# Optimization experiments

Measured on AMD Instinct MI355X. Metric: run time of the kernel, lower is better.

The kernel has to match this reference:

```python
import jax, jax.numpy as jnp
import numpy as np

N_NODES = 10000
N_EDGES = 640000
D = 128
N_GRAPHS = 16
N_CLASSES = 10


def setup_inputs() -> dict:
    key = jax.random.key(0)
    ks = jax.random.split(key, 12)
    x = jax.random.normal(ks[0], (N_NODES, D), dtype=jnp.float32)
    edge_index = jax.random.randint(ks[1], (2, N_EDGES), 0, N_NODES, dtype=jnp.int64)
    batch_ids = jnp.sort(jax.random.randint(ks[2], (N_NODES,), 0, N_GRAPHS, dtype=jnp.int64))
    s = 1.0 / np.sqrt(D)
    W_in = jax.random.normal(ks[3], (D, D), dtype=jnp.float32) * s
    W_self = jax.random.normal(ks[4], (D, D), dtype=jnp.float32) * s
    b = jnp.zeros((D,), dtype=jnp.float32)
    W_e1 = jax.random.normal(ks[5], (2 * D, D), dtype=jnp.float32) * (1.0 / np.sqrt(2 * D))
    b_e1 = jnp.zeros((D,), dtype=jnp.float32)
    W_e2 = jax.random.normal(ks[6], (D, 1), dtype=jnp.float32) * s
    b_e2 = jnp.zeros((1,), dtype=jnp.float32)
    W_cls = jax.random.normal(ks[7], (D, N_CLASSES), dtype=jnp.float32) * s
    b_cls = jnp.zeros((N_CLASSES,), dtype=jnp.float32)
    return {"x": x, "edge_index": edge_index, "batch_ids": batch_ids,
            "W_in": W_in, "W_self": W_self, "b": b,
            "W_e1": W_e1, "b_e1": b_e1, "W_e2": W_e2, "b_e2": b_e2,
            "W_cls": W_cls, "b_cls": b_cls}


def reference(x, edge_index, batch_ids, W_in, W_self, b, W_e1, b_e1, W_e2, b_e2, W_cls, b_cls):
    src, dst = edge_index[0], edge_index[1]
    # --- gnn(data) -> (z_node, z_graph) : GCN-style message passing ---
    h = x @ W_in                                  # [N, D]
    agg = jax.ops.segment_sum(h[src], dst, num_segments=N_NODES)  # [N, D]
    z_node = jax.nn.relu(agg + x @ W_self + b)    # [N, D]
    # mean pool per graph -> z_graph [B, D]
    sums = jax.ops.segment_sum(z_node, batch_ids, num_segments=N_GRAPHS)
    counts = jax.ops.segment_sum(jnp.ones((N_NODES,), dtype=z_node.dtype), batch_ids, num_segments=N_GRAPHS)
    z_graph = sums / jnp.maximum(counts, 1.0)[:, None]
    # --- edge predictor: gather, concat, MLP ---
    edge_features = jnp.concatenate([z_node[src], z_node[dst]], axis=1)  # [E, 2D]
    pred_edge = jax.nn.relu(edge_features @ W_e1 + b_e1) @ W_e2 + b_e2   # [E, 1]
    # --- classifier ---
    pred_class = z_graph @ W_cls + b_cls          # [B, n_classes]
    return (pred_edge, pred_class)
```

## Files before the change

### kernel.cpp

```cpp
#include <hip/hip_runtime.h>

#define N_NODES   10000
#define N_EDGES   640000
#define DIM       128
#define N_GRAPHS  16
#define N_CLASSES 10

typedef unsigned int uint;
typedef unsigned short ushort;

__device__ __forceinline__ float bf2f(uint lo16) {
    return __uint_as_float(lo16 << 16);
}
__device__ __forceinline__ ushort f2bf(float f) {
    uint u = __float_as_uint(f);
    u += 0x7fffu + ((u >> 16) & 1u);
    return (ushort)(u >> 16);
}

__global__ __launch_bounds__(256) void conv_bf16(
    const float* __restrict__ x, uint* __restrict__ xb)
{
    const int idx = blockIdx.x * 256 + threadIdx.x;
    const float4 v = ((const float4*)x)[idx];
    uint lo = (uint)f2bf(v.x) | ((uint)f2bf(v.y) << 16);
    uint hi = (uint)f2bf(v.z) | ((uint)f2bf(v.w) << 16);
    ((uint2*)xb)[idx] = make_uint2(lo, hi);
}

__global__ __launch_bounds__(256) void hist_dst(
    const int* __restrict__ dst, int* __restrict__ cnt)
{
    const int base = (blockIdx.x * 256 + threadIdx.x) * 4;
    const int d0 = dst[base + 0];
    const int d1 = dst[base + 1];
    const int d2 = dst[base + 2];
    const int d3 = dst[base + 3];
    atomicAdd(&cnt[d0], 1);
    atomicAdd(&cnt[d1], 1);
    atomicAdd(&cnt[d2], 1);
    atomicAdd(&cnt[d3], 1);
}

__global__ __launch_bounds__(256) void count_nodes(
    const int* __restrict__ bid, float* __restrict__ gcnt)
{
    __shared__ int h[N_GRAPHS];
    const int t = threadIdx.x;
    if (t < N_GRAPHS) h[t] = 0;
    __syncthreads();
    for (int n = t; n < N_NODES; n += 256) atomicAdd(&h[bid[n]], 1);
    __syncthreads();
    if (t < N_GRAPHS) gcnt[t] = (float)h[t];
}

__global__ __launch_bounds__(1024) void scan_k(
    const int* __restrict__ cnt, int* __restrict__ cursor)
{
    __shared__ int s[1024];
    const int t = threadIdx.x;
    int local[10];
    int sum = 0;
    if (t < 1000) {
        for (int j = 0; j < 10; ++j) { local[j] = sum; sum += cnt[t * 10 + j]; }
    }
    s[t] = (t < 1000) ? sum : 0;
    __syncthreads();
    for (int st = 1; st < 1024; st <<= 1) {
        int v = (t >= st) ? s[t - st] : 0;
        __syncthreads();
        s[t] += v;
        __syncthreads();
    }
    if (t < 1000) {
        const int off = (t == 0) ? 0 : s[t - 1];
        for (int j = 0; j < 10; ++j) cursor[t * 10 + j] = off + local[j];
    }
}

__global__ __launch_bounds__(256) void fill_csr(
    const int* __restrict__ src, const int* __restrict__ dst,
    int* __restrict__ cursor, uint* __restrict__ srcs)
{
    const int base = (blockIdx.x * 256 + threadIdx.x) * 4;
    const int d0 = dst[base + 0];
    const int d1 = dst[base + 1];
    const int d2 = dst[base + 2];
    const int d3 = dst[base + 3];
    const int s0 = src[base + 0];
    const int s1 = src[base + 1];
    const int s2 = src[base + 2];
    const int s3 = src[base + 3];
    const int p0 = atomicAdd(&cursor[d0], 1);
    const int p1 = atomicAdd(&cursor[d1], 1);
    const int p2 = atomicAdd(&cursor[d2], 1);
    const int p3 = atomicAdd(&cursor[d3], 1);
    srcs[p0] = (uint)s0;
    srcs[p1] = (uint)s1;
    srcs[p2] = (uint)s2;
    srcs[p3] = (uint)s3;
}

__global__ __launch_bounds__(256) void gather_xb(
    const uint* __restrict__ xb,
    const int* __restrict__ cnt, const int* __restrict__ cursor,
    const uint* __restrict__ srcs,
    float* __restrict__ XAGG)
{
    const int n    = blockIdx.x * 4 + (threadIdx.x >> 6);
    const int lane = threadIdx.x & 63;
    const int end  = cursor[n];
    int i = end - cnt[n];

    float a0 = 0.f, b0 = 0.f, a1 = 0.f, b1 = 0.f;
    float a2 = 0.f, b2 = 0.f, a3 = 0.f, b3 = 0.f;

    for (; i + 4 <= end; i += 4) {
        const uint s0 = srcs[i], s1 = srcs[i + 1], s2 = srcs[i + 2], s3 = srcs[i + 3];
        const uint v0 = xb[s0 * 64 + lane];
        const uint v1 = xb[s1 * 64 + lane];
        const uint v2 = xb[s2 * 64 + lane];
        const uint v3 = xb[s3 * 64 + lane];
        a0 += bf2f(v0 & 0xffffu); b0 += bf2f(v0 >> 16);
        a1 += bf2f(v1 & 0xffffu); b1 += bf2f(v1 >> 16);
        a2 += bf2f(v2 & 0xffffu); b2 += bf2f(v2 >> 16);
        a3 += bf2f(v3 & 0xffffu); b3 += bf2f(v3 >> 16);
    }
    for (; i < end; ++i) {
        const uint v = xb[srcs[i] * 64 + lane];
        a0 += bf2f(v & 0xffffu); b0 += bf2f(v >> 16);
    }
    float2 s;
    s.x = (a0 + a1) + (a2 + a3);
    s.y = (b0 + b1) + (b2 + b3);
    *(float2*)&XAGG[n * DIM + lane * 2] = s;
}

__global__ __launch_bounds__(256) void gemm_zu(
    const float* __restrict__ XAGG_in, const float* __restrict__ x,
    const float* __restrict__ W_in, const float* __restrict__ W_self,
    const float* __restrict__ b, const int* __restrict__ bid,
    const float* __restrict__ W_e1, const float* __restrict__ b_e1,
    float* __restrict__ gsum, ushort* __restrict__ U12)
{
    __shared__ float sa[16 * DIM];
    __shared__ float sb[16 * DIM];
    __shared__ int sbid[16];
    const int base = blockIdx.x * 16;
    const int t = threadIdx.x;
    {
        const float4* ga = (const float4*)(XAGG_in + base * DIM);
        const float4* gb = (const float4*)(x + base * DIM);
        float4* la = (float4*)sa;
        float4* lb = (float4*)sb;
        for (int i = t; i < 16 * DIM / 4; i += 256) { la[i] = ga[i]; lb[i] = gb[i]; }
        if (t < 16) sbid[t] = bid[base + t];
    }
    __syncthreads();

    const int half = t >> 7, c = t & 127;

    {
        const float* __restrict__ W = half ? W_self : W_in;
        const float4* A4 = (const float4*)(half ? sb : sa);
        float acc[16];
#pragma unroll
        for (int r = 0; r < 16; ++r) acc[r] = 0.f;
        for (int k4 = 0; k4 < DIM / 4; ++k4) {
            const float w0 = W[(k4 * 4 + 0) * DIM + c];
            const float w1 = W[(k4 * 4 + 1) * DIM + c];
            const float w2 = W[(k4 * 4 + 2) * DIM + c];
            const float w3 = W[(k4 * 4 + 3) * DIM + c];
#pragma unroll
            for (int r = 0; r < 16; ++r) {
                const float4 xv = A4[r * (DIM / 4) + k4];
                acc[r] = fmaf(xv.x, w0, acc[r]);
                acc[r] = fmaf(xv.y, w1, acc[r]);
                acc[r] = fmaf(xv.z, w2, acc[r]);
                acc[r] = fmaf(xv.w, w3, acc[r]);
            }
        }
        __syncthreads();
        if (half) {
#pragma unroll
            for (int r = 0; r < 16; ++r) sb[r * DIM + c] = acc[r];
        }
        __syncthreads();
        if (!half) {
            const float bv = b[c];
            float run = 0.f;
            int cur = sbid[0];
#pragma unroll
            for (int r = 0; r < 16; ++r) {
                const float z = fmaxf(acc[r] + sb[r * DIM + c] + bv, 0.f);
                sa[r * DIM + c] = z;
                const int g = sbid[r];
                if (g != cur) { unsafeAtomicAdd(&gsum[cur * DIM + c], run); run = 0.f; cur = g; }
                run += z;
            }
            unsafeAtomicAdd(&gsum[cur * DIM + c], run);
        }
        __syncthreads();
    }

    {
        const float* __restrict__ W = W_e1 + half * 128 * DIM;
        const float4* Z4 = (const float4*)sa;
        float acc[16];
#pragma unroll
        for (int r = 0; r < 16; ++r) acc[r] = 0.f;
        for (int k4 = 0; k4 < DIM / 4; ++k4) {
            const float w0 = W[(k4 * 4 + 0) * DIM + c];
            const float w1 = W[(k4 * 4 + 1) * DIM + c];
            const float w2 = W[(k4 * 4 + 2) * DIM + c];
            const float w3 = W[(k4 * 4 + 3) * DIM + c];
#pragma unroll
            for (int r = 0; r < 16; ++r) {
                const float4 xv = Z4[r * (DIM / 4) + k4];
                acc[r] = fmaf(xv.x, w0, acc[r]);
                acc[r] = fmaf(xv.y, w1, acc[r]);
                acc[r] = fmaf(xv.z, w2, acc[r]);
                acc[r] = fmaf(xv.w, w3, acc[r]);
            }
        }
        const float bv = half ? 0.f : b_e1[c];
        for (int r = 0; r < 16; ++r)
            U12[(base + r) * 256 + half * 128 + c] = f2bf(acc[r] + bv);
    }
}

__device__ __forceinline__ void ch2(uint a, uint b, float wl, float wh,
                                    float& accl, float& acch)
{
    const float fl = fmaxf(__uint_as_float(a << 16) + __uint_as_float(b << 16), 0.f);
    const float fh = fmaxf(__uint_as_float(a & 0xffff0000u) + __uint_as_float(b & 0xffff0000u), 0.f);
    accl = fmaf(fl, wl, accl);
    acch = fmaf(fh, wh, acch);
}

__global__ __launch_bounds__(256) void edge_mlp3(
    const ushort* __restrict__ U12,
    const int* __restrict__ src, const int* __restrict__ dst,
    const float* __restrict__ W_e2, const float* __restrict__ b_e2,
    float* __restrict__ out)
{
    __shared__ float ws[DIM];
    const int t = threadIdx.x;
    if (t < DIM) ws[t] = W_e2[t];
    __syncthreads();

    const int l16  = t & 15;
    const int grp  = t >> 4;
    const int e    = blockIdx.x * 16 + grp;

    const int s = src[e];
    const int d = dst[e];

    const uint4 a  = *(const uint4*)(U12 + s * 256 + l16 * 8);
    const uint4 bv = *(const uint4*)(U12 + d * 256 + 128 + l16 * 8);
    const float4 w0 = ((const float4*)ws)[l16 * 2 + 0];
    const float4 w1 = ((const float4*)ws)[l16 * 2 + 1];

    float acc0 = 0.f, acc1 = 0.f;
    ch2(a.x, bv.x, w0.x, w0.y, acc0, acc1);
    ch2(a.y, bv.y, w0.z, w0.w, acc0, acc1);
    ch2(a.z, bv.z, w1.x, w1.y, acc0, acc1);
    ch2(a.w, bv.w, w1.z, w1.w, acc0, acc1);

    float p = acc0 + acc1;
#pragma unroll
    for (int off = 8; off >= 1; off >>= 1)
        p += __shfl_xor(p, off);

    if (l16 == 0) out[e] = p + b_e2[0];
}

__global__ __launch_bounds__(256) void classify(
    const float* __restrict__ gsum, const float* __restrict__ gcnt,
    const float* __restrict__ W_cls, const float* __restrict__ b_cls,
    float* __restrict__ out)
{
    const int t = threadIdx.x;
    if (t >= N_GRAPHS * N_CLASSES) return;
    const int g = t / N_CLASSES;
    const int c = t % N_CLASSES;
    const float inv = 1.0f / fmaxf(gcnt[g], 1.0f);
    float acc = 0.f;
    for (int k = 0; k < DIM; ++k)
        acc += gsum[g * DIM + k] * W_cls[k * N_CLASSES + c];
    out[g * N_CLASSES + c] = acc * inv + b_cls[c];
}

extern "C" void kernel_launch(void* const* d_in, const int* in_sizes, int n_in,
                              void* d_out, int out_size, void* d_ws, size_t ws_size,
                              hipStream_t stream)
{
    const float* x      = (const float*)d_in[0];
    const int*   eidx   = (const int*)  d_in[1];
    const int*   bid    = (const int*)  d_in[2];
    const float* W_in   = (const float*)d_in[3];
    const float* W_self = (const float*)d_in[4];
    const float* b      = (const float*)d_in[5];
    const float* W_e1   = (const float*)d_in[6];
    const float* b_e1   = (const float*)d_in[7];
    const float* W_e2   = (const float*)d_in[8];
    const float* b_e2   = (const float*)d_in[9];
    const float* W_cls  = (const float*)d_in[10];
    const float* b_cls  = (const float*)d_in[11];
    float* out = (float*)d_out;

    char* ws = (char*)d_ws;
    int*    cnt    = (int*)   (ws);
    float*  gsum   = (float*) (ws + 40960);
    float*  gcnt   = (float*) (ws + 49152);
    int*    cursor = (int*)   (ws + 65536);
    uint*   srcs   = (uint*)  (ws + 131072);
    float*  XAGG   = (float*) (ws + 131072 + 2560000);
    ushort* U12    = (ushort*)(ws + 131072 + 7680000);
    uint*   xb     = (uint*)  (ws + 131072 + 12800000);

    const int* src = eidx;
    const int* dst = eidx + N_EDGES;

    hipMemsetAsync(d_ws, 0, 65536, stream);

    conv_bf16  <<<(N_NODES * DIM / 4) / 256, 256, 0, stream>>>(x, xb);
    hist_dst   <<<N_EDGES / 1024, 256, 0, stream>>>(dst, cnt);
    count_nodes<<<1, 256, 0, stream>>>(bid, gcnt);
    scan_k     <<<1, 1024, 0, stream>>>(cnt, cursor);
    fill_csr   <<<N_EDGES / 1024, 256, 0, stream>>>(src, dst, cursor, srcs);
    gather_xb  <<<N_NODES / 4, 256, 0, stream>>>(xb, cnt, cursor, srcs, XAGG);
    gemm_zu    <<<N_NODES / 16, 256, 0, stream>>>(XAGG, x, W_in, W_self, b, bid,
                                                  W_e1, b_e1, gsum, U12);
    edge_mlp3  <<<N_EDGES / 16, 256, 0, stream>>>(U12, src, dst, W_e2, b_e2, out);
    classify   <<<1, 256, 0, stream>>>(gsum, gcnt, W_cls, b_cls, out + N_EDGES);
}
```

Baseline: 280.9 us.

## Traverse edges in dst-sorted CSR order for edge MLP and shrink gemm tile

fill_csr now stores (src, original edge id) pairs, and the edge MLP runs per destination node. It loads the node's U2 row once and walks its incoming edges, writing each result scattered back to the original edge index. The aim is to drop the random dst-row gather and get reuse of U2. The gather loop is unrolled to 8, and gemm_zu uses 8 rows per block for more blocks. The costs are a doubled index array, scattered output writes, and per-node load imbalance with only 625 blocks in the edge kernel.

```diff
diff --git a/kernel.cpp b/kernel.cpp
--- a/kernel.cpp
+++ b/kernel.cpp
@@ -80,7 +80,7 @@
 
 __global__ __launch_bounds__(256) void fill_csr(
     const int* __restrict__ src, const int* __restrict__ dst,
-    int* __restrict__ cursor, uint* __restrict__ srcs)
+    int* __restrict__ cursor, uint2* __restrict__ pairs)
 {
     const int base = (blockIdx.x * 256 + threadIdx.x) * 4;
     const int d0 = dst[base + 0];
@@ -95,16 +95,16 @@
     const int p1 = atomicAdd(&cursor[d1], 1);
     const int p2 = atomicAdd(&cursor[d2], 1);
     const int p3 = atomicAdd(&cursor[d3], 1);
-    srcs[p0] = (uint)s0;
-    srcs[p1] = (uint)s1;
-    srcs[p2] = (uint)s2;
-    srcs[p3] = (uint)s3;
+    pairs[p0] = make_uint2((uint)s0, (uint)(base + 0));
+    pairs[p1] = make_uint2((uint)s1, (uint)(base + 1));
+    pairs[p2] = make_uint2((uint)s2, (uint)(base + 2));
+    pairs[p3] = make_uint2((uint)s3, (uint)(base + 3));
 }
 
 __global__ __launch_bounds__(256) void gather_xb(
     const uint* __restrict__ xb,
     const int* __restrict__ cnt, const int* __restrict__ cursor,
-    const uint* __restrict__ srcs,
+    const uint2* __restrict__ pairs,
     float* __restrict__ XAGG)
 {
     const int n    = blockIdx.x * 4 + (threadIdx.x >> 6);
@@ -115,19 +115,26 @@
     float a0 = 0.f, b0 = 0.f, a1 = 0.f, b1 = 0.f;
     float a2 = 0.f, b2 = 0.f, a3 = 0.f, b3 = 0.f;
 
-    for (; i + 4 <= end; i += 4) {
-        const uint s0 = srcs[i], s1 = srcs[i + 1], s2 = srcs[i + 2], s3 = srcs[i + 3];
-        const uint v0 = xb[s0 * 64 + lane];
-        const uint v1 = xb[s1 * 64 + lane];
-        const uint v2 = xb[s2 * 64 + lane];
-        const uint v3 = xb[s3 * 64 + lane];
+    for (; i + 8 <= end; i += 8) {
+        const uint v0 = xb[pairs[i + 0].x * 64 + lane];
+        const uint v1 = xb[pairs[i + 1].x * 64 + lane];
+        const uint v2 = xb[pairs[i + 2].x * 64 + lane];
+        const uint v3 = xb[pairs[i + 3].x * 64 + lane];
+        const uint v4 = xb[pairs[i + 4].x * 64 + lane];
+        const uint v5 = xb[pairs[i + 5].x * 64 + lane];
+        const uint v6 = xb[pairs[i + 6].x * 64 + lane];
+        const uint v7 = xb[pairs[i + 7].x * 64 + lane];
         a0 += bf2f(v0 & 0xffffu); b0 += bf2f(v0 >> 16);
         a1 += bf2f(v1 & 0xffffu); b1 += bf2f(v1 >> 16);
         a2 += bf2f(v2 & 0xffffu); b2 += bf2f(v2 >> 16);
         a3 += bf2f(v3 & 0xffffu); b3 += bf2f(v3 >> 16);
+        a0 += bf2f(v4 & 0xffffu); b0 += bf2f(v4 >> 16);
+        a1 += bf2f(v5 & 0xffffu); b1 += bf2f(v5 >> 16);
+        a2 += bf2f(v6 & 0xffffu); b2 += bf2f(v6 >> 16);
+        a3 += bf2f(v7 & 0xffffu); b3 += bf2f(v7 >> 16);
     }
     for (; i < end; ++i) {
-        const uint v = xb[srcs[i] * 64 + lane];
+        const uint v = xb[pairs[i].x * 64 + lane];
         a0 += bf2f(v & 0xffffu); b0 += bf2f(v >> 16);
     }
     float2 s;
@@ -136,6 +143,7 @@
     *(float2*)&XAGG[n * DIM + lane * 2] = s;
 }
 
+#define ZROWS 8
 __global__ __launch_bounds__(256) void gemm_zu(
     const float* __restrict__ XAGG_in, const float* __restrict__ x,
     const float* __restrict__ W_in, const float* __restrict__ W_self,
@@ -143,18 +151,18 @@
     const float* __restrict__ W_e1, const float* __restrict__ b_e1,
     float* __restrict__ gsum, ushort* __restrict__ U12)
 {
-    __shared__ float sa[16 * DIM];
-    __shared__ float sb[16 * DIM];
-    __shared__ int sbid[16];
-    const int base = blockIdx.x * 16;
+    __shared__ float sa[ZROWS * DIM];
+    __shared__ float sb[ZROWS * DIM];
+    __shared__ int sbid[ZROWS];
+    const int base = blockIdx.x * ZROWS;
     const int t = threadIdx.x;
     {
         const float4* ga = (const float4*)(XAGG_in + base * DIM);
         const float4* gb = (const float4*)(x + base * DIM);
         float4* la = (float4*)sa;
         float4* lb = (float4*)sb;
-        for (int i = t; i < 16 * DIM / 4; i += 256) { la[i] = ga[i]; lb[i] = gb[i]; }
-        if (t < 16) sbid[t] = bid[base + t];
+        for (int i = t; i < ZROWS * DIM / 4; i += 256) { la[i] = ga[i]; lb[i] = gb[i]; }
+        if (t < ZROWS) sbid[t] = bid[base + t];
     }
     __syncthreads();
 
@@ -163,16 +171,16 @@
     {
         const float* __restrict__ W = half ? W_self : W_in;
         const float4* A4 = (const float4*)(half ? sb : sa);
-        float acc[16];
-#pragma unroll
-        for (int r = 0; r < 16; ++r) acc[r] = 0.f;
+        float acc[ZROWS];
+#pragma unroll
+        for (int r = 0; r < ZROWS; ++r) acc[r] = 0.f;
         for (int k4 = 0; k4 < DIM / 4; ++k4) {
             const float w0 = W[(k4 * 4 + 0) * DIM + c];
             const float w1 = W[(k4 * 4 + 1) * DIM + c];
             const float w2 = W[(k4 * 4 + 2) * DIM + c];
             const float w3 = W[(k4 * 4 + 3) * DIM + c];
 #pragma unroll
-            for (int r = 0; r < 16; ++r) {
+            for (int r = 0; r < ZROWS; ++r) {
                 const float4 xv = A4[r * (DIM / 4) + k4];
                 acc[r] = fmaf(xv.x, w0, acc[r]);
                 acc[r] = fmaf(xv.y, w1, acc[r]);
@@ -183,7 +191,7 @@
         __syncthreads();
         if (half) {
 #pragma unroll
-            for (int r = 0; r < 16; ++r) sb[r * DIM + c] = acc[r];
+            for (int r = 0; r < ZROWS; ++r) sb[r * DIM + c] = acc[r];
         }
         __syncthreads();
         if (!half) {
@@ -191,7 +199,7 @@
             float run = 0.f;
             int cur = sbid[0];
 #pragma unroll
-            for (int r = 0; r < 16; ++r) {
+            for (int r = 0; r < ZROWS; ++r) {
                 const float z = fmaxf(acc[r] + sb[r * DIM + c] + bv, 0.f);
                 sa[r * DIM + c] = z;
                 const int g = sbid[r];
@@ -206,16 +214,16 @@
     {
         const float* __restrict__ W = W_e1 + half * 128 * DIM;
         const float4* Z4 = (const float4*)sa;
-        float acc[16];
-#pragma unroll
-        for (int r = 0; r < 16; ++r) acc[r] = 0.f;
+        float acc[ZROWS];
+#pragma unroll
+        for (int r = 0; r < ZROWS; ++r) acc[r] = 0.f;
         for (int k4 = 0; k4 < DIM / 4; ++k4) {
             const float w0 = W[(k4 * 4 + 0) * DIM + c];
             const float w1 = W[(k4 * 4 + 1) * DIM + c];
             const float w2 = W[(k4 * 4 + 2) * DIM + c];
             const float w3 = W[(k4 * 4 + 3) * DIM + c];
 #pragma unroll
-            for (int r = 0; r < 16; ++r) {
+            for (int r = 0; r < ZROWS; ++r) {
                 const float4 xv = Z4[r * (DIM / 4) + k4];
                 acc[r] = fmaf(xv.x, w0, acc[r]);
                 acc[r] = fmaf(xv.y, w1, acc[r]);
@@ -224,7 +232,7 @@
             }
         }
         const float bv = half ? 0.f : b_e1[c];
-        for (int r = 0; r < 16; ++r)
+        for (int r = 0; r < ZROWS; ++r)
             U12[(base + r) * 256 + half * 128 + c] = f2bf(acc[r] + bv);
     }
 }
@@ -238,9 +246,10 @@
     acch = fmaf(fh, wh, acch);
 }
 
-__global__ __launch_bounds__(256) void edge_mlp3(
+__global__ __launch_bounds__(256) void edge_mlp4(
     const ushort* __restrict__ U12,
-    const int* __restrict__ src, const int* __restrict__ dst,
+    const int* __restrict__ cnt, const int* __restrict__ cursor,
+    const uint2* __restrict__ pairs,
     const float* __restrict__ W_e2, const float* __restrict__ b_e2,
     float* __restrict__ out)
 {
@@ -249,30 +258,55 @@
     if (t < DIM) ws[t] = W_e2[t];
     __syncthreads();
 
-    const int l16  = t & 15;
-    const int grp  = t >> 4;
-    const int e    = blockIdx.x * 16 + grp;
-
-    const int s = src[e];
-    const int d = dst[e];
-
-    const uint4 a  = *(const uint4*)(U12 + s * 256 + l16 * 8);
-    const uint4 bv = *(const uint4*)(U12 + d * 256 + 128 + l16 * 8);
+    const int l16 = t & 15;
+    const int grp = t >> 4;
+    const int n   = blockIdx.x * 16 + grp;
+
+    const int end = cursor[n];
+    int i = end - cnt[n];
+
+    const uint4 u2 = *(const uint4*)(U12 + n * 256 + 128 + l16 * 8);
     const float4 w0 = ((const float4*)ws)[l16 * 2 + 0];
     const float4 w1 = ((const float4*)ws)[l16 * 2 + 1];
-
-    float acc0 = 0.f, acc1 = 0.f;
-    ch2(a.x, bv.x, w0.x, w0.y, acc0, acc1);
-    ch2(a.y, bv.y, w0.z, w0.w, acc0, acc1);
-    ch2(a.z, bv.z, w1.x, w1.y, acc0, acc1);
-    ch2(a.w, bv.w, w1.z, w1.w, acc0, acc1);
-
-    float p = acc0 + acc1;
-#pragma unroll
-    for (int off = 8; off >= 1; off >>= 1)
-        p += __shfl_xor(p, off);
-
-    if (l16 == 0) out[e] = p + b_e2[0];
+    const float be2 = b_e2[0];
+
+    for (; i + 2 <= end; i += 2) {
+        const uint2 pa = pairs[i];
+        const uint2 pb = pairs[i + 1];
+        const uint4 A = *(const uint4*)(U12 + pa.x * 256 + l16 * 8);
+        const uint4 B = *(const uint4*)(U12 + pb.x * 256 + l16 * 8);
+        float p0 = 0.f, p1 = 0.f, q0 = 0.f, q1 = 0.f;
+        ch2(A.x, u2.x, w0.x, w0.y, p0, p1);
+        ch2(A.y, u2.y, w0.z, w0.w, p0, p1);
+        ch2(A.z, u2.z, w1.x, w1.y, p0, p1);
+        ch2(A.w, u2.w, w1.z, w1.w, p0, p1);
+        ch2(B.x, u2.x, w0.x, w0.y, q0, q1);
+        ch2(B.y, u2.y, w0.z, w0.w, q0, q1);
+        ch2(B.z, u2.z, w1.x, w1.y, q0, q1);
+        ch2(B.w, u2.w, w1.z, w1.w, q0, q1);
+        float p = p0 + p1;
+        float q = q0 + q1;
+#pragma unroll
+        for (int off = 8; off >= 1; off >>= 1) {
+            p += __shfl_xor(p, off);
+            q += __shfl_xor(q, off);
+        }
+        if (l16 == 0) { out[pa.y] = p + be2; out[pb.y] = q + be2; }
+    }
+    if (i < end) {
+        const uint2 pa = pairs[i];
+        const uint4 A = *(const uint4*)(U12 + pa.x * 256 + l16 * 8);
+        float p0 = 0.f, p1 = 0.f;
+        ch2(A.x, u2.x, w0.x, w0.y, p0, p1);
+        ch2(A.y, u2.y, w0.z, w0.w, p0, p1);
+        ch2(A.z, u2.z, w1.x, w1.y, p0, p1);
+        ch2(A.w, u2.w, w1.z, w1.w, p0, p1);
+        float p = p0 + p1;
+#pragma unroll
+        for (int off = 8; off >= 1; off >>= 1)
+            p += __shfl_xor(p, off);
+        if (l16 == 0) out[pa.y] = p + be2;
+    }
 }
 
 __global__ __launch_bounds__(256) void classify(
@@ -314,10 +348,10 @@
     float*  gsum   = (float*) (ws + 40960);
     float*  gcnt   = (float*) (ws + 49152);
     int*    cursor = (int*)   (ws + 65536);
-    uint*   srcs   = (uint*)  (ws + 131072);
-    float*  XAGG   = (float*) (ws + 131072 + 2560000);
-    ushort* U12    = (ushort*)(ws + 131072 + 7680000);
-    uint*   xb     = (uint*)  (ws + 131072 + 12800000);
+    uint2*  pairs  = (uint2*) (ws + 131072);
+    float*  XAGG   = (float*) (ws + 131072 + 5120000);
+    ushort* U12    = (ushort*)(ws + 131072 + 10240000);
+    uint*   xb     = (uint*)  (ws + 131072 + 15360000);
 
     const int* src = eidx;
     const int* dst = eidx + N_EDGES;
@@ -328,10 +362,10 @@
     hist_dst   <<<N_EDGES / 1024, 256, 0, stream>>>(dst, cnt);
     count_nodes<<<1, 256, 0, stream>>>(bid, gcnt);
     scan_k     <<<1, 1024, 0, stream>>>(cnt, cursor);
-    fill_csr   <<<N_EDGES / 1024, 256, 0, stream>>>(src, dst, cursor, srcs);
-    gather_xb  <<<N_NODES / 4, 256, 0, stream>>>(xb, cnt, cursor, srcs, XAGG);
-    gemm_zu    <<<N_NODES / 16, 256, 0, stream>>>(XAGG, x, W_in, W_self, b, bid,
-                                                  W_e1, b_e1, gsum, U12);
-    edge_mlp3  <<<N_EDGES / 16, 256, 0, stream>>>(U12, src, dst, W_e2, b_e2, out);
+    fill_csr   <<<N_EDGES / 1024, 256, 0, stream>>>(src, dst, cursor, pairs);
+    gather_xb  <<<N_NODES / 4, 256, 0, stream>>>(xb, cnt, cursor, pairs, XAGG);
+    gemm_zu    <<<N_NODES / ZROWS, 256, 0, stream>>>(XAGG, x, W_in, W_self, b, bid,
+                                                     W_e1, b_e1, gsum, U12);
+    edge_mlp4  <<<N_NODES / 16, 256, 0, stream>>>(U12, cnt, cursor, pairs, W_e2, b_e2, out);
     classify   <<<1, 256, 0, stream>>>(gsum, gcnt, W_cls, b_cls, out + N_EDGES);
 }
```

New measurement: 282.4 us. About the same (+0.5%).
